# Kernel optimization log

Measured on AMD Instinct MI355X. Metric: run time of the kernel, lower is better.

Reference implementation:

```python
import jax, jax.numpy as jnp
import numpy as np

B, C_IN, H, W = 8, 1024, 18, 80
FEAT = 1024
A = 32      # anchors per location
NCLS = 3    # classes
NREG = 13
K = 3       # kernel size
K2 = K * K
EPS = 1e-5  # BatchNorm eps


def conv2d(x, w, b):
    y = jax.lax.conv_general_dilated(x, w, (1, 1), ((1, 1), (1, 1)),
                                     dimension_numbers=('NCHW', 'OIHW', 'NCHW'))
    return y + b[None, :, None, None]


def bn_eval(x, g, b):
    # eval-mode BatchNorm2d with running_mean=0, running_var=1
    return x * (g / jnp.sqrt(1.0 + EPS))[None, :, None, None] + b[None, :, None, None]


def anchor_flatten(x, d):
    # [B, A*d, H, W] -> permute(0,2,3,1) -> [B, H*W*A, d]
    Bx, Cx, Hx, Wx = x.shape
    return jnp.transpose(x, (0, 2, 3, 1)).reshape(Bx, Hx * Wx * (Cx // d), d)


def bilinear_gather(x, py, px):
    # x: [B,C,H,W]; py/px: [B,K2,H,W] float coords -> [B,C,K2,H,W], zero outside
    Bx, Cx, Hx, Wx = x.shape
    y0 = jnp.floor(py); x0 = jnp.floor(px)
    wy1 = py - y0; wx1 = px - x0
    wy0 = 1.0 - wy1; wx0 = 1.0 - wx1
    xf = x.reshape(Bx, Cx, Hx * Wx)

    def g(yy, xx):
        valid = ((yy >= 0) & (yy < Hx) & (xx >= 0) & (xx < Wx)).astype(x.dtype)
        yc = jnp.clip(yy, 0, Hx - 1).astype(jnp.int32)
        xc = jnp.clip(xx, 0, Wx - 1).astype(jnp.int32)
        idx = (yc * Wx + xc).reshape(Bx, -1)
        vals = jax.vmap(lambda xi, ii: xi[:, ii])(xf, idx).reshape(Bx, Cx, K2, Hx, Wx)
        return vals * valid[:, None]

    return (g(y0, x0) * (wy0 * wx0)[:, None] + g(y0, x0 + 1) * (wy0 * wx1)[:, None]
            + g(y0 + 1, x0) * (wy1 * wx0)[:, None] + g(y0 + 1, x0 + 1) * (wy1 * wx1)[:, None])


def mdcn(x, off_w, off_b, w, b):
    # ModulatedDeformConvPack (DCNv2): 3x3 conv -> (dy, dx, mask), then modulated deform conv
    out = conv2d(x, off_w, off_b)                        # [B, 3*K2, H, W]
    dy, dx, m = out[:, :K2], out[:, K2:2 * K2], jax.nn.sigmoid(out[:, 2 * K2:])
    ky, kx = jnp.meshgrid(jnp.arange(K, dtype=x.dtype), jnp.arange(K, dtype=x.dtype), indexing='ij')
    base_y = jnp.arange(x.shape[2], dtype=x.dtype)[None, None, :, None] - 1.0 + ky.reshape(1, K2, 1, 1)
    base_x = jnp.arange(x.shape[3], dtype=x.dtype)[None, None, None, :] - 1.0 + kx.reshape(1, K2, 1, 1)
    sampled = bilinear_gather(x, base_y + dy, base_x + dx) * m[:, None]   # [B,C,K2,H,W]
    O = w.shape[0]
    return jnp.einsum('bckhw,ock->bohw', sampled, w.reshape(O, w.shape[1], K2)) + b[None, :, None, None]


def setup_inputs() -> dict:
    key = jax.random.key(0)
    ks = jax.random.split(key, 10)
    s1 = 1.0 / np.sqrt(C_IN * K2)
    s2 = 1.0 / np.sqrt(FEAT * K2)
    rn = lambda k, sh, sc: jax.random.normal(k, sh, jnp.float32) * sc
    return {
        'features': jax.random.normal(ks[0], (B, C_IN, H, W), jnp.float32),
        'cls_w1': rn(ks[1], (FEAT, C_IN, K, K), s1), 'cls_b1': jnp.zeros((FEAT,), jnp.float32),
        'cls_w2': rn(ks[2], (FEAT, FEAT, K, K), s2), 'cls_b2': jnp.zeros((FEAT,), jnp.float32),
        'cls_w3': rn(ks[3], (A * NCLS, FEAT, K, K), s2), 'cls_b3': jnp.zeros((A * NCLS,), jnp.float32),
        'off_w': rn(ks[4], (3 * K2, C_IN, K, K), s1), 'off_b': jnp.zeros((3 * K2,), jnp.float32),
        'dcn_w': rn(ks[5], (FEAT, C_IN, K, K), s1), 'dcn_b': jnp.zeros((FEAT,), jnp.float32),
        'bn1_g': jnp.ones((FEAT,), jnp.float32), 'bn1_b': jnp.zeros((FEAT,), jnp.float32),
        'reg_w2': rn(ks[6], (FEAT, FEAT, K, K), s2), 'reg_b2': jnp.zeros((FEAT,), jnp.float32),
        'bn2_g': jnp.ones((FEAT,), jnp.float32), 'bn2_b': jnp.zeros((FEAT,), jnp.float32),
        'reg_w3': rn(ks[7], (A * NREG, FEAT, K, K), s2), 'reg_b3': jnp.zeros((A * NREG,), jnp.float32),
    }


def reference(features, cls_w1, cls_b1, cls_w2, cls_b2, cls_w3, cls_b3,
              off_w, off_b, dcn_w, dcn_b, bn1_g, bn1_b,
              reg_w2, reg_b2, bn2_g, bn2_b, reg_w3, reg_b3):
    # cls branch (Dropout2d is identity in eval)
    h = jax.nn.relu(conv2d(features, cls_w1, cls_b1))
    h = jax.nn.relu(conv2d(h, cls_w2, cls_b2))
    cls_preds = anchor_flatten(conv2d(h, cls_w3, cls_b3), NCLS)   # [B, H*W*A, NCLS]
    # reg branch: modulated deformable conv -> BN -> ReLU -> conv -> BN -> ReLU -> conv
    r = jax.nn.relu(bn_eval(mdcn(features, off_w, off_b, dcn_w, dcn_b), bn1_g, bn1_b))
    r = jax.nn.relu(bn_eval(conv2d(r, reg_w2, reg_b2), bn2_g, bn2_b))
    reg_preds = anchor_flatten(conv2d(r, reg_w3, reg_b3), NREG)   # [B, H*W*A, NREG]
    return (cls_preds, reg_preds)
```

## Files before the change

### kernel.cpp

```cpp
#include <hip/hip_runtime.h>
#include <math.h>

typedef short short8 __attribute__((ext_vector_type(8)));
typedef float f32x4 __attribute__((ext_vector_type(4)));
typedef unsigned short u16;
typedef unsigned int u32;

#define GAS(p) ((__attribute__((address_space(1))) void*)(p))
#define LAS(p) ((__attribute__((address_space(3))) void*)(p))

namespace {

constexpr int HW   = 1440;
constexpr int PBAT = 20 * 82 * 1024;

__device__ __forceinline__ u16 f2bf(float f) {
  u32 u = __float_as_uint(f);
  return (u16)((u + 0x7FFFu + ((u >> 16) & 1u)) >> 16);
}
__device__ __forceinline__ float bf2f(u16 h) {
  return __uint_as_float(((u32)h) << 16);
}

__global__ __launch_bounds__(256)
void transpose_feat(const float* __restrict__ src, u16* __restrict__ dst) {
  __shared__ float tile[128][17];
  const int bh = blockIdx.y;
  const int b = bh / 18, h = bh % 18;
  const int wt = blockIdx.x % 5, ct = blockIdx.x / 5;
  const int w0 = wt * 16, c0 = ct * 128;
  const int tid = threadIdx.x;
#pragma unroll
  for (int it = 0; it < 8; ++it) {
    int idx = it * 256 + tid;
    int c = idx >> 4, w = idx & 15;
    tile[c][w] = src[((size_t)(b * 1024 + c0 + c) * 18 + h) * 80 + w0 + w];
  }
  __syncthreads();
  const int px = tid >> 4, cq = tid & 15;
  union { uint4 u; u16 s[8]; } pk;
#pragma unroll
  for (int j = 0; j < 8; ++j) pk.s[j] = f2bf(tile[cq * 8 + j][px]);
  *(uint4*)(dst + ((size_t)(b * 20 + h + 1) * 82 + (w0 + px + 1)) * 1024 + c0 + cq * 8) = pk.u;
}

struct RepackArgs {
  const float* src[7];
  u16* dst[7];
  int O[7];
  int start[7];
  int nseg;
};

__global__ __launch_bounds__(256)
void repack_all(RepackArgs ra) {
  int blk = blockIdx.x;
  int seg = 0;
#pragma unroll
  for (int i = 1; i < 7; ++i)
    if (i < ra.nseg && blk >= ra.start[i]) seg = i;
  const float* src = ra.src[seg];
  u16* dst = ra.dst[seg];
  const int O = ra.O[seg];
  int idx = (blk - ra.start[seg]) * 256 + threadIdx.x;
  if (idx >= O * 128) return;
  int o = idx >> 7, c8 = idx & 127;
  const float* s = src + (size_t)o * 9216 + (size_t)c8 * 72;
  float v[72];
#pragma unroll
  for (int i = 0; i < 18; ++i) {
    float4 f = *(const float4*)(s + i * 4);
    v[i * 4 + 0] = f.x; v[i * 4 + 1] = f.y; v[i * 4 + 2] = f.z; v[i * 4 + 3] = f.w;
  }
#pragma unroll
  for (int t = 0; t < 9; ++t) {
    union { uint4 u; u16 h[8]; } pk;
#pragma unroll
    for (int j = 0; j < 8; ++j) pk.h[j] = f2bf(v[j * 9 + t]);
    *(uint4*)(dst + ((size_t)t * O + o) * 1024 + c8 * 8) = pk.u;
  }
}

__device__ __forceinline__
void sample_body(int k, int lp, int pix0, int Npc,
                 const u16* __restrict__ featP, const float* __restrict__ offp,
                 u16* __restrict__ spl, int tid) {
  const int p = pix0 + lp;
  const int c8 = tid & 15;
  int b = p / HW, hw = p - b * HW;
  int h = hw / 80, w = hw - h * 80;
  float dy = offp[p * 27 + k];
  float dx = offp[p * 27 + 9 + k];
  float ml = offp[p * 27 + 18 + k];
  float m = 1.f / (1.f + expf(-ml));
  float py = (float)(h - 1 + k / 3) + dy;
  float px = (float)(w - 1 + (k % 3)) + dx;
  float y0f = floorf(py), x0f = floorf(px);
  float wy1 = py - y0f, wx1 = px - x0f;
  float wy0 = 1.f - wy1, wx0 = 1.f - wx1;
  int y0 = (int)y0f, x0 = (int)x0f;
  int ya = min(max(y0, -1), 18),  yb = min(max(y0 + 1, -1), 18);
  int xa = min(max(x0, -1), 80),  xb = min(max(x0 + 1, -1), 80);
  const u16* base = featP + (size_t)b * PBAT;
  const u16* r00 = base + ((size_t)(ya + 1) * 82 + (xa + 1)) * 1024;
  const u16* r01 = base + ((size_t)(ya + 1) * 82 + (xb + 1)) * 1024;
  const u16* r10 = base + ((size_t)(yb + 1) * 82 + (xa + 1)) * 1024;
  const u16* r11 = base + ((size_t)(yb + 1) * 82 + (xb + 1)) * 1024;
  float w00 = wy0 * wx0 * m, w01 = wy0 * wx1 * m;
  float w10 = wy1 * wx0 * m, w11 = wy1 * wx1 * m;
  u16* dst = spl + ((size_t)k * Npc + lp) * 1024;
  for (int c = c8 * 8; c < 1024; c += 128) {
    union { uint4 u; u16 h[8]; } a, bq, cq2, d, o;
    a.u   = *(const uint4*)(r00 + c);
    bq.u  = *(const uint4*)(r01 + c);
    cq2.u = *(const uint4*)(r10 + c);
    d.u   = *(const uint4*)(r11 + c);
#pragma unroll
    for (int j = 0; j < 8; ++j) {
      float v = w00 * bf2f(a.h[j]) + w01 * bf2f(bq.h[j]) +
                w10 * bf2f(cq2.h[j]) + w11 * bf2f(d.h[j]);
      o.h[j] = f2bf(v);
    }
    *(uint4*)(dst + c) = o.u;
  }
}

__global__ __launch_bounds__(256)
void sample_standalone(const u16* __restrict__ featP, const float* __restrict__ offp,
                       u16* __restrict__ spl, int pix0, int Npc) {
  sample_body(blockIdx.y, blockIdx.x * 16 + (threadIdx.x >> 4), pix0, Npc,
              featP, offp, spl, threadIdx.x);
}

template<int PLANES, int STOREF32, int HASBN, int HASRELU>
__global__ __launch_bounds__(256)
void mfma_conv(const u16* __restrict__ W, const u16* __restrict__ Bp,
               const float* __restrict__ bias, const float* __restrict__ bng,
               const float* __restrict__ bnb, void* __restrict__ outv,
               int Co, int pix0, int Npc) {
  __shared__ __align__(16) u16 As[128 * 32];
  __shared__ __align__(16) u16 Bs[128 * 32];
  const int tid = threadIdx.x;
  const int wv = tid >> 6, lane = tid & 63;
  const int o0 = blockIdx.y * 128;
  const int p0 = pix0 + blockIdx.x * 128;

  const int lr = lane >> 2;
  const int qs = (lane & 3) ^ ((lane >> 3) & 3);
  int aoff[2], boff[2];
#pragma unroll
  for (int s = 0; s < 2; ++s) {
    int r = (wv * 2 + s) * 16 + lr;
    int o = min(o0 + r, Co - 1);
    aoff[s] = o * 1024 + qs * 8;
    int p = p0 + r;
    if (PLANES) {
      boff[s] = (p - pix0) * 1024 + qs * 8;
    } else {
      int b = p / HW, hw = p - b * HW;
      int h = hw / 80, w = hw - h * 80;
      boff[s] = ((b * 20 + h) * 82 + w) * 1024 + qs * 8;
    }
  }
  u16* aDst = As + (wv * 2) * 512;
  u16* bDst = Bs + (wv * 2) * 512;

  const int wm = wv >> 1, wn = wv & 1;
  const int frm = lane & 15;
  const int kq = lane >> 4;
  const int sel = (kq ^ ((lane >> 1) & 3)) * 16;

  f32x4 acc[4][4];
#pragma unroll
  for (int i = 0; i < 4; ++i)
#pragma unroll
    for (int j = 0; j < 4; ++j) acc[i][j] = (f32x4)0.f;

  for (int t = 0; t < 9; ++t) {
    const u16* Wt = W + (size_t)t * Co * 1024;
    const u16* Bt = Bp + (PLANES ? (size_t)t * (size_t)Npc * 1024
                                 : (size_t)(((t / 3) * 82 + (t % 3)) * 1024));
    for (int cc = 0; cc < 1024; cc += 32) {
      __syncthreads();
#pragma unroll
      for (int s = 0; s < 2; ++s) {
        __builtin_amdgcn_global_load_lds(GAS(Wt + aoff[s] + cc), LAS(aDst + s * 512), 16, 0, 0);
        __builtin_amdgcn_global_load_lds(GAS(Bt + boff[s] + cc), LAS(bDst + s * 512), 16, 0, 0);
      }
      __syncthreads();
      uint4 af[4], bf4[4];
#pragma unroll
      for (int i = 0; i < 4; ++i) {
        af[i]  = *(const uint4*)((const char*)As + (wm * 64 + i * 16 + frm) * 64 + sel);
        bf4[i] = *(const uint4*)((const char*)Bs + (wn * 64 + i * 16 + frm) * 64 + sel);
      }
#pragma unroll
      for (int i = 0; i < 4; ++i) {
        short8 a = __builtin_bit_cast(short8, af[i]);
#pragma unroll
        for (int j = 0; j < 4; ++j) {
          short8 b = __builtin_bit_cast(short8, bf4[j]);
          acc[i][j] = __builtin_amdgcn_mfma_f32_16x16x32_bf16(a, b, acc[i][j], 0, 0, 0);
        }
      }
    }
  }

  size_t obase[4];
#pragma unroll
  for (int j = 0; j < 4; ++j) {
    int pn = p0 + wn * 64 + j * 16 + frm;
    if (STOREF32) {
      obase[j] = (size_t)pn * Co;
    } else {
      int b = pn / HW, hw = pn - b * HW;
      int h = hw / 80, w = hw - h * 80;
      obase[j] = ((size_t)(b * 20 + h + 1) * 82 + (w + 1)) * 1024;
    }
  }
#pragma unroll
  for (int i = 0; i < 4; ++i) {
    int o = o0 + wm * 64 + i * 16 + kq * 4;
    float bi[4], sc[4], sh[4];
#pragma unroll
    for (int r = 0; r < 4; ++r) {
      int oc = min(o + r, Co - 1);
      bi[r] = bias[oc];
      if (HASBN) { sc[r] = bng[oc] * rsqrtf(1.f + 1e-5f); sh[r] = bnb[oc]; }
    }
#pragma unroll
    for (int j = 0; j < 4; ++j) {
      float v[4];
#pragma unroll
      for (int r = 0; r < 4; ++r) {
        float x = acc[i][j][r] + bi[r];
        if (HASBN) x = x * sc[r] + sh[r];
        if (HASRELU) x = fmaxf(x, 0.f);
        v[r] = x;
      }
      if (STOREF32) {
        float* op = (float*)outv;
#pragma unroll
        for (int r = 0; r < 4; ++r)
          if (o + r < Co) op[obase[j] + o + r] = v[r];
      } else {
        u16* op = (u16*)outv;
        ushort4 pk;
        pk.x = f2bf(v[0]); pk.y = f2bf(v[1]); pk.z = f2bf(v[2]); pk.w = f2bf(v[3]);
        *(ushort4*)(op + obase[j] + o) = pk;
      }
    }
  }
}

__global__ __launch_bounds__(256)
void gemm_sample(const u16* __restrict__ W, const u16* __restrict__ Bp,
                 const float* __restrict__ bias, void* __restrict__ outv, int Co,
                 const u16* __restrict__ featP, const float* __restrict__ offp,
                 u16* __restrict__ spl, int gemmBlocks) {
  __shared__ __align__(16) u16 As[128 * 32];
  __shared__ __align__(16) u16 Bs[128 * 32];
  const int gx = blockIdx.x;
  const int tid = threadIdx.x;
  if (gx >= gemmBlocks) {
    int sidx = gx - gemmBlocks;
    int k = sidx / 720, bs = sidx % 720;
    sample_body(k, bs * 16 + (tid >> 4), 0, 11520, featP, offp, spl, tid);
    return;
  }
  const int wv = tid >> 6, lane = tid & 63;
  const int o0 = (gx / 90) * 128;
  const int p0 = (gx % 90) * 128;

  const int lr = lane >> 2;
  const int qs = (lane & 3) ^ ((lane >> 3) & 3);
  int aoff[2], boff[2];
#pragma unroll
  for (int s = 0; s < 2; ++s) {
    int r = (wv * 2 + s) * 16 + lr;
    int o = min(o0 + r, Co - 1);
    aoff[s] = o * 1024 + qs * 8;
    int p = p0 + r;
    int b = p / HW, hw = p - b * HW;
    int h = hw / 80, w = hw - h * 80;
    boff[s] = ((b * 20 + h) * 82 + w) * 1024 + qs * 8;
  }
  u16* aDst = As + (wv * 2) * 512;
  u16* bDst = Bs + (wv * 2) * 512;

  const int wm = wv >> 1, wn = wv & 1;
  const int frm = lane & 15;
  const int kq = lane >> 4;
  const int sel = (kq ^ ((lane >> 1) & 3)) * 16;

  f32x4 acc[4][4];
#pragma unroll
  for (int i = 0; i < 4; ++i)
#pragma unroll
    for (int j = 0; j < 4; ++j) acc[i][j] = (f32x4)0.f;

  for (int t = 0; t < 9; ++t) {
    const u16* Wt = W + (size_t)t * Co * 1024;
    const u16* Bt = Bp + (size_t)(((t / 3) * 82 + (t % 3)) * 1024);
    for (int cc = 0; cc < 1024; cc += 32) {
      __syncthreads();
#pragma unroll
      for (int s = 0; s < 2; ++s) {
        __builtin_amdgcn_global_load_lds(GAS(Wt + aoff[s] + cc), LAS(aDst + s * 512), 16, 0, 0);
        __builtin_amdgcn_global_load_lds(GAS(Bt + boff[s] + cc), LAS(bDst + s * 512), 16, 0, 0);
      }
      __syncthreads();
      uint4 af[4], bf4[4];
#pragma unroll
      for (int i = 0; i < 4; ++i) {
        af[i]  = *(const uint4*)((const char*)As + (wm * 64 + i * 16 + frm) * 64 + sel);
        bf4[i] = *(const uint4*)((const char*)Bs + (wn * 64 + i * 16 + frm) * 64 + sel);
      }
#pragma unroll
      for (int i = 0; i < 4; ++i) {
        short8 a = __builtin_bit_cast(short8, af[i]);
#pragma unroll
        for (int j = 0; j < 4; ++j) {
          short8 b = __builtin_bit_cast(short8, bf4[j]);
          acc[i][j] = __builtin_amdgcn_mfma_f32_16x16x32_bf16(a, b, acc[i][j], 0, 0, 0);
        }
      }
    }
  }

  size_t obase[4];
#pragma unroll
  for (int j = 0; j < 4; ++j) {
    int pn = p0 + wn * 64 + j * 16 + frm;
    int b = pn / HW, hw = pn - b * HW;
    int h = hw / 80, w = hw - h * 80;
    obase[j] = ((size_t)(b * 20 + h + 1) * 82 + (w + 1)) * 1024;
  }
#pragma unroll
  for (int i = 0; i < 4; ++i) {
    int o = o0 + wm * 64 + i * 16 + kq * 4;
    float bi[4];
#pragma unroll
    for (int r = 0; r < 4; ++r) bi[r] = bias[min(o + r, Co - 1)];
#pragma unroll
    for (int j = 0; j < 4; ++j) {
      u16* op = (u16*)outv;
      ushort4 pk;
      pk.x = f2bf(fmaxf(acc[i][j][0] + bi[0], 0.f));
      pk.y = f2bf(fmaxf(acc[i][j][1] + bi[1], 0.f));
      pk.z = f2bf(fmaxf(acc[i][j][2] + bi[2], 0.f));
      pk.w = f2bf(fmaxf(acc[i][j][3] + bi[3], 0.f));
      *(ushort4*)(op + obase[j] + o) = pk;
    }
  }
}

}

extern "C" void kernel_launch(void* const* d_in, const int* in_sizes, int n_in,
                              void* d_out, int out_size, void* d_ws, size_t ws_size,
                              hipStream_t stream) {
  const float* feat   = (const float*)d_in[0];
  const float* cls_w1 = (const float*)d_in[1];
  const float* cls_b1 = (const float*)d_in[2];
  const float* cls_w2 = (const float*)d_in[3];
  const float* cls_b2 = (const float*)d_in[4];
  const float* cls_w3 = (const float*)d_in[5];
  const float* cls_b3 = (const float*)d_in[6];
  const float* off_w  = (const float*)d_in[7];
  const float* off_b  = (const float*)d_in[8];
  const float* dcn_w  = (const float*)d_in[9];
  const float* dcn_b  = (const float*)d_in[10];
  const float* bn1_g  = (const float*)d_in[11];
  const float* bn1_b  = (const float*)d_in[12];
  const float* reg_w2 = (const float*)d_in[13];
  const float* reg_b2 = (const float*)d_in[14];
  const float* bn2_g  = (const float*)d_in[15];
  const float* bn2_b  = (const float*)d_in[16];
  const float* reg_w3 = (const float*)d_in[17];
  const float* reg_b3 = (const float*)d_in[18];
  float* outp = (float*)d_out;

  const size_t ACTB = 26869760;
  char* wsb = (char*)d_ws;
  u16* featP = (u16*)(wsb);
  u16* bufA  = (u16*)(wsb + ACTB);
  u16* bufB  = (u16*)(wsb + 2 * ACTB);
  u16* wts   = (u16*)(wsb + 3 * ACTB);
  float* offp = (float*)(wsb + 3 * ACTB + 85432320);
  u16* spl   = (u16*)(wsb + 3 * ACTB + 85432320 + 1244160);
  const size_t BASE = 3 * ACTB + 85432320 + 1244160;
  const size_t SPLB = (size_t)9 * 11520 * 1024 * 2;

  u16* offT = wts;
  u16* w1T  = wts + 248832;
  u16* w2T  = wts + 9686016;
  u16* w3T  = wts + 19123200;
  u16* dcnT = wts + 20007936;
  u16* r2T  = wts + 29445120;
  u16* r3T  = wts + 38882304;

  dim3 blk(256);

  hipMemsetAsync(featP, 0, 3 * ACTB, stream);
  transpose_feat<<<dim3(40, 144), blk, 0, stream>>>(feat, featP);

  {
    RepackArgs ra;
    const float* s[7] = {off_w, cls_w1, cls_w2, cls_w3, dcn_w, reg_w2, reg_w3};
    u16* d[7] = {offT, w1T, w2T, w3T, dcnT, r2T, r3T};
    int  O[7] = {27, 1024, 1024, 96, 1024, 1024, 416};
    int acc = 0;
    for (int i = 0; i < 7; ++i) {
      ra.src[i] = s[i]; ra.dst[i] = d[i]; ra.O[i] = O[i]; ra.start[i] = acc;
      acc += (O[i] * 128 + 255) / 256;
    }
    ra.nseg = 7;
    repack_all<<<dim3(acc), blk, 0, stream>>>(ra);
  }

  mfma_conv<0, 1, 0, 0><<<dim3(90, 1), blk, 0, stream>>>(
      offT, featP, off_b, nullptr, nullptr, offp, 27, 0, 0);

  mfma_conv<0, 0, 0, 1><<<dim3(90, 8), blk, 0, stream>>>(
      w1T, featP, cls_b1, nullptr, nullptr, bufA, 1024, 0, 0);

  if (ws_size >= BASE + SPLB) {
    gemm_sample<<<dim3(720 + 6480), blk, 0, stream>>>(
        w2T, bufA, cls_b2, bufB, 1024, featP, offp, spl, 720);
    mfma_conv<1, 0, 1, 1><<<dim3(90, 8), blk, 0, stream>>>(
        dcnT, spl, dcn_b, bn1_g, bn1_b, featP, 1024, 0, 11520);
    mfma_conv<0, 1, 0, 0><<<dim3(90, 1), blk, 0, stream>>>(
        w3T, bufB, cls_b3, nullptr, nullptr, outp, 96, 0, 0);
    mfma_conv<0, 0, 1, 1><<<dim3(90, 8), blk, 0, stream>>>(
        r2T, featP, reg_b2, bn2_g, bn2_b, bufA, 1024, 0, 0);
    mfma_conv<0, 1, 0, 0><<<dim3(90, 4), blk, 0, stream>>>(
        r3T, bufA, reg_b3, nullptr, nullptr, outp + 1105920, 416, 0, 0);
  } else {
    mfma_conv<0, 0, 0, 1><<<dim3(90, 8), blk, 0, stream>>>(
        w2T, bufA, cls_b2, nullptr, nullptr, bufB, 1024, 0, 0);
    size_t avail = ws_size > BASE ? ws_size - BASE : 0;
    int tiles = (int)(avail / 2359296);
    if (tiles < 1) tiles = 1;
    if (tiles > 90) tiles = 90;
    for (int t0 = 0; t0 < 90; t0 += tiles) {
      int nt = (90 - t0) < tiles ? (90 - t0) : tiles;
      int pix0 = t0 * 128, np = nt * 128;
      sample_standalone<<<dim3(nt * 8, 9), blk, 0, stream>>>(featP, offp, spl, pix0, np);
      mfma_conv<1, 0, 1, 1><<<dim3(nt, 8), blk, 0, stream>>>(
          dcnT, spl, dcn_b, bn1_g, bn1_b, bufA, 1024, pix0, np);
    }
    mfma_conv<0, 1, 0, 0><<<dim3(90, 1), blk, 0, stream>>>(
        w3T, bufB, cls_b3, nullptr, nullptr, outp, 96, 0, 0);
    mfma_conv<0, 0, 1, 1><<<dim3(90, 8), blk, 0, stream>>>(
        r2T, bufA, reg_b2, bn2_g, bn2_b, featP, 1024, 0, 0);
    mfma_conv<0, 1, 0, 0><<<dim3(90, 4), blk, 0, stream>>>(
        r3T, featP, reg_b3, nullptr, nullptr, outp + 1105920, 416, 0, 0);
  }
}
```

Baseline: 2.185 ms.

## Split-K over taps with atomic accumulation for small-output convolutions

Adds a split-K convolution kernel that partitions the 9 filter taps across blocks and accumulates fp32 results with atomicAdd. The thin-output convs (offset conv with 27 channels, cls head with 96, reg head with 416) otherwise launched only 90 or 360 blocks, under-filling the GPU. The outputs are zeroed with memsets first. The cls head conv is also moved earlier in the stream, right after the gemm_sample launch. The cost is atomic traffic on the outputs, extra memsets, and non-deterministic summation order.

```diff
diff --git a/kernel.cpp b/kernel.cpp
--- a/kernel.cpp
+++ b/kernel.cpp
@@ -254,6 +254,96 @@
 }
 
 __global__ __launch_bounds__(256)
+void mfma_conv_sk(const u16* __restrict__ W, const u16* __restrict__ Bp,
+                  const float* __restrict__ bias, float* __restrict__ out,
+                  int Co, int tapsPerGrp) {
+  __shared__ __align__(16) u16 As[128 * 32];
+  __shared__ __align__(16) u16 Bs[128 * 32];
+  const int tid = threadIdx.x;
+  const int wv = tid >> 6, lane = tid & 63;
+  const int px = blockIdx.x % 90;
+  const int t0 = (blockIdx.x / 90) * tapsPerGrp;
+  const int t1 = t0 + tapsPerGrp;
+  const int o0 = blockIdx.y * 128;
+  const int p0 = px * 128;
+
+  const int lr = lane >> 2;
+  const int qs = (lane & 3) ^ ((lane >> 3) & 3);
+  int aoff[2], boff[2];
+#pragma unroll
+  for (int s = 0; s < 2; ++s) {
+    int r = (wv * 2 + s) * 16 + lr;
+    int o = min(o0 + r, Co - 1);
+    aoff[s] = o * 1024 + qs * 8;
+    int p = p0 + r;
+    int b = p / HW, hw = p - b * HW;
+    int h = hw / 80, w = hw - h * 80;
+    boff[s] = ((b * 20 + h) * 82 + w) * 1024 + qs * 8;
+  }
+  u16* aDst = As + (wv * 2) * 512;
+  u16* bDst = Bs + (wv * 2) * 512;
+
+  const int wm = wv >> 1, wn = wv & 1;
+  const int frm = lane & 15;
+  const int kq = lane >> 4;
+  const int sel = (kq ^ ((lane >> 1) & 3)) * 16;
+
+  f32x4 acc[4][4];
+#pragma unroll
+  for (int i = 0; i < 4; ++i)
+#pragma unroll
+    for (int j = 0; j < 4; ++j) acc[i][j] = (f32x4)0.f;
+
+  for (int t = t0; t < t1; ++t) {
+    const u16* Wt = W + (size_t)t * Co * 1024;
+    const u16* Bt = Bp + (size_t)(((t / 3) * 82 + (t % 3)) * 1024);
+    for (int cc = 0; cc < 1024; cc += 32) {
+      __syncthreads();
+#pragma unroll
+      for (int s = 0; s < 2; ++s) {
+        __builtin_amdgcn_global_load_lds(GAS(Wt + aoff[s] + cc), LAS(aDst + s * 512), 16, 0, 0);
+        __builtin_amdgcn_global_load_lds(GAS(Bt + boff[s] + cc), LAS(bDst + s * 512), 16, 0, 0);
+      }
+      __syncthreads();
+      uint4 af[4], bf4[4];
+#pragma unroll
+      for (int i = 0; i < 4; ++i) {
+        af[i]  = *(const uint4*)((const char*)As + (wm * 64 + i * 16 + frm) * 64 + sel);
+        bf4[i] = *(const uint4*)((const char*)Bs + (wn * 64 + i * 16 + frm) * 64 + sel);
+      }
+#pragma unroll
+      for (int i = 0; i < 4; ++i) {
+        short8 a = __builtin_bit_cast(short8, af[i]);
+#pragma unroll
+        for (int j = 0; j < 4; ++j) {
+          short8 b = __builtin_bit_cast(short8, bf4[j]);
+          acc[i][j] = __builtin_amdgcn_mfma_f32_16x16x32_bf16(a, b, acc[i][j], 0, 0, 0);
+        }
+      }
+    }
+  }
+
+  const bool addBias = (t0 == 0);
+  size_t obase[4];
+#pragma unroll
+  for (int j = 0; j < 4; ++j) obase[j] = (size_t)(p0 + wn * 64 + j * 16 + frm) * Co;
+#pragma unroll
+  for (int i = 0; i < 4; ++i) {
+    int o = o0 + wm * 64 + i * 16 + kq * 4;
+    float bi[4];
+#pragma unroll
+    for (int r = 0; r < 4; ++r) bi[r] = addBias ? bias[min(o + r, Co - 1)] : 0.f;
+#pragma unroll
+    for (int j = 0; j < 4; ++j) {
+#pragma unroll
+      for (int r = 0; r < 4; ++r) {
+        if (o + r < Co) atomicAdd(&out[obase[j] + o + r], acc[i][j][r] + bi[r]);
+      }
+    }
+  }
+}
+
+__global__ __launch_bounds__(256)
 void gemm_sample(const u16* __restrict__ W, const u16* __restrict__ Bp,
                  const float* __restrict__ bias, void* __restrict__ outv, int Co,
                  const u16* __restrict__ featP, const float* __restrict__ offp,
@@ -403,6 +493,8 @@
   dim3 blk(256);
 
   hipMemsetAsync(featP, 0, 3 * ACTB, stream);
+  hipMemsetAsync(offp, 0, 1244160, stream);
+  hipMemsetAsync(d_out, 0, (size_t)out_size * 4, stream);
   transpose_feat<<<dim3(40, 144), blk, 0, stream>>>(feat, featP);
 
   {
@@ -419,8 +511,7 @@
     repack_all<<<dim3(acc), blk, 0, stream>>>(ra);
   }
 
-  mfma_conv<0, 1, 0, 0><<<dim3(90, 1), blk, 0, stream>>>(
-      offT, featP, off_b, nullptr, nullptr, offp, 27, 0, 0);
+  mfma_conv_sk<<<dim3(810, 1), blk, 0, stream>>>(offT, featP, off_b, offp, 27, 1);
 
   mfma_conv<0, 0, 0, 1><<<dim3(90, 8), blk, 0, stream>>>(
       w1T, featP, cls_b1, nullptr, nullptr, bufA, 1024, 0, 0);
@@ -428,14 +519,13 @@
   if (ws_size >= BASE + SPLB) {
     gemm_sample<<<dim3(720 + 6480), blk, 0, stream>>>(
         w2T, bufA, cls_b2, bufB, 1024, featP, offp, spl, 720);
+    mfma_conv_sk<<<dim3(810, 1), blk, 0, stream>>>(w3T, bufB, cls_b3, outp, 96, 1);
     mfma_conv<1, 0, 1, 1><<<dim3(90, 8), blk, 0, stream>>>(
         dcnT, spl, dcn_b, bn1_g, bn1_b, featP, 1024, 0, 11520);
-    mfma_conv<0, 1, 0, 0><<<dim3(90, 1), blk, 0, stream>>>(
-        w3T, bufB, cls_b3, nullptr, nullptr, outp, 96, 0, 0);
     mfma_conv<0, 0, 1, 1><<<dim3(90, 8), blk, 0, stream>>>(
         r2T, featP, reg_b2, bn2_g, bn2_b, bufA, 1024, 0, 0);
-    mfma_conv<0, 1, 0, 0><<<dim3(90, 4), blk, 0, stream>>>(
-        r3T, bufA, reg_b3, nullptr, nullptr, outp + 1105920, 416, 0, 0);
+    mfma_conv_sk<<<dim3(270, 4), blk, 0, stream>>>(
+        r3T, bufA, reg_b3, outp + 1105920, 416, 3);
   } else {
     mfma_conv<0, 0, 0, 1><<<dim3(90, 8), blk, 0, stream>>>(
         w2T, bufA, cls_b2, nullptr, nullptr, bufB, 1024, 0, 0);
@@ -450,11 +540,10 @@
       mfma_conv<1, 0, 1, 1><<<dim3(nt, 8), blk, 0, stream>>>(
           dcnT, spl, dcn_b, bn1_g, bn1_b, bufA, 1024, pix0, np);
     }
-    mfma_conv<0, 1, 0, 0><<<dim3(90, 1), blk, 0, stream>>>(
-        w3T, bufB, cls_b3, nullptr, nullptr, outp, 96, 0, 0);
+    mfma_conv_sk<<<dim3(810, 1), blk, 0, stream>>>(w3T, bufB, cls_b3, outp, 96, 1);
     mfma_conv<0, 0, 1, 1><<<dim3(90, 8), blk, 0, stream>>>(
         r2T, bufA, reg_b2, bn2_g, bn2_b, featP, 1024, 0, 0);
-    mfma_conv<0, 1, 0, 0><<<dim3(90, 4), blk, 0, stream>>>(
-        r3T, featP, reg_b3, nullptr, nullptr, outp + 1105920, 416, 0, 0);
-  }
-}
+    mfma_conv_sk<<<dim3(270, 4), blk, 0, stream>>>(
+        r3T, featP, reg_b3, outp + 1105920, 416, 3);
+  }
+}
```

Measured after the change: 2.259 ms. 3.4% more time.
